# Kernel tuning notes

Hardware: AMD Instinct MI355X
Metric: run time of the kernel (lower is better)

The kernel has to match this reference:

```python
import jax, jax.numpy as jnp
import numpy as np

HIDDEN = 256
BLUR_RADIUS = 3  # truncate gaussian (std=1.0) at 3 sigma -> 7-tap separable kernel


def _gauss_kernel(std=1.0):
    t = jnp.arange(-BLUR_RADIUS, BLUR_RADIUS + 1, dtype=jnp.float32)
    k = jnp.exp(-0.5 * (t / std) ** 2)
    return k / k.sum()


def _blur_axis(vol, k, axis):
    # vol: [B,D,D,D]; separable 1D conv along `axis` (1..3), SAME padding
    v = jnp.moveaxis(vol, axis, -1)
    shp = v.shape
    v = v.reshape(-1, 1, shp[-1])
    out = jax.lax.conv_general_dilated(v, k.reshape(1, 1, -1), (1,), 'SAME')
    return jnp.moveaxis(out.reshape(shp), -1, axis)


def low_pass_3d(vol, std=1.0):
    k = _gauss_kernel(std).astype(vol.dtype)
    for ax in (1, 2, 3):
        vol = _blur_axis(vol, k, ax)
    return vol


def generate_sphere_points(n, rng):
    phi = rng.uniform(0, 2 * np.pi, n)
    cos_theta = rng.uniform(-1, 1, n)
    theta = np.arccos(cos_theta)
    r = rng.uniform(0, 1, n) ** (1.0 / 3.0)
    return np.stack([r * np.sin(theta) * np.cos(phi),
                     r * np.sin(theta) * np.sin(phi),
                     r * np.cos(theta)], axis=-1)


def setup_inputs() -> dict:
    key = jax.random.key(0)
    B, LAT, V, D = 8, 128, 65536, 128
    ks = list(jax.random.split(key, 16))
    rng = np.random.default_rng(0)

    def siren_first(k, fan_in, fan_out):
        lim = 1.0 / fan_in
        return jax.random.uniform(k, (fan_in, fan_out), jnp.float32, -lim, lim)

    def siren(k, fan_in, fan_out, c=6.0):
        lim = np.sqrt(c / fan_in) / 30.0
        return jax.random.uniform(k, (fan_in, fan_out), jnp.float32, -lim, lim)

    def head(k, fan_in, fan_out):
        # variance_scaling(scale=1/3, mode=fan_out, uniform)
        lim = np.sqrt(3.0 * (1.0 / 3.0) / fan_out)
        return jax.random.uniform(k, (fan_in, fan_out), jnp.float32, -lim, lim)

    inp = {
        'x': jax.random.normal(ks[0], (B, LAT), jnp.float32),
        'w0': siren_first(ks[1], LAT, HIDDEN), 'b0': jnp.zeros((HIDDEN,), jnp.float32),
        'w1': siren(ks[2], HIDDEN, HIDDEN), 'b1': jnp.zeros((HIDDEN,), jnp.float32),
        'w2': siren(ks[3], HIDDEN, HIDDEN), 'b2': jnp.zeros((HIDDEN,), jnp.float32),
        'w3': siren(ks[4], HIDDEN, HIDDEN), 'b3': jnp.zeros((HIDDEN,), jnp.float32),
        'w4': siren(ks[5], HIDDEN, HIDDEN), 'b4': jnp.zeros((HIDDEN,), jnp.float32),
        'wc': head(ks[6], HIDDEN, 3 * V), 'bc': jnp.zeros((3 * V,), jnp.float32),
        'wv': head(ks[7], HIDDEN, V), 'bv': jnp.zeros((V,), jnp.float32),
        'coords0': jnp.asarray(0.25 * (generate_sphere_points(V, rng) + rng.normal(0, 0.1, (V, 3))), jnp.float32),
        'values0': jnp.zeros((V,), jnp.float32),
        'volume_size': D,
    }
    return inp


# corner offsets, ordered as in the original concat: 000,100,010,001,011,101,110,111 (x,y,z)
_OFFSETS = jnp.array([[0, 0, 0], [1, 0, 0], [0, 1, 0], [0, 0, 1],
                      [0, 1, 1], [1, 0, 1], [1, 1, 0], [1, 1, 1]], dtype=jnp.int32)


def reference(x, w0, b0, w1, b1, w2, b2, w3, b3, w4, b4, wc, bc, wv, bv,
              coords0, values0, volume_size):
    B = x.shape[0]
    V = values0.shape[0]
    D = volume_size
    factor = 0.5 * D
    bf = jnp.bfloat16

    # --- SIREN MLP (hidden layers computed in bf16, heads in fp32) ---
    h = jnp.sin(30.0 * (x.astype(bf) @ w0.astype(bf) + b0.astype(bf)))
    for w, b in ((w1, b1), (w2, b2), (w3, b3)):
        h = jnp.sin(h + (h @ w.astype(bf) + b.astype(bf)))
    h = h @ w4.astype(bf) + b4.astype(bf)
    h = h.astype(jnp.float32)

    delta_coords = (h @ wc + bc).reshape(B, V, 3)
    values = jax.nn.relu(values0[None, :] + (h @ wv + bv))  # [B,V]

    coords = factor * (coords0[None] + delta_coords) + factor  # [B,V,3], voxel units

    # --- trilinear splatting ---
    bposf = jnp.floor(coords)
    bposi = bposf.astype(jnp.int32)              # [B,V,3]
    f = coords - bposf                           # fractional part, [B,V,3]
    # weight per corner: prod_d (f_d if offset else 1-f_d) -> [B,V,8]
    w8 = jnp.prod(jnp.where(_OFFSETS[None, None].astype(bool), f[:, :, None, :], 1.0 - f[:, :, None, :]), axis=-1)
    amp = values[:, :, None] * w8                # [B,V,8]
    idx = bposi[:, :, None, :] + _OFFSETS[None, None]  # [B,V,8,3] (x,y,z)
    # linear index with (z,y,x) layout as in original scatter
    lin = (idx[..., 2] * D + idx[..., 1]) * D + idx[..., 0]  # [B,V,8]

    def scatter_one(lin_b, amp_b):
        return jnp.zeros((D * D * D,), jnp.float32).at[lin_b.ravel()].add(amp_b.ravel())

    grids = jax.vmap(scatter_one)(lin, amp).reshape(B, D, D, D)

    # --- gaussian low-pass, std=1.0 ---
    grids = low_pass_3d(grids, std=1.0)
    return grids
```

## Files before the change

### kernel.cpp

```cpp
#include <hip/hip_runtime.h>
#include <hip/hip_bf16.h>

#define DD 128
#define D3 (DD*DD*DD)
#define NB 8
#define NV 65536
#define HID 256
#define LAT 128

#define NBIN 2048
#define NBIN_TOT (NBIN*NB)
#define NMASK 512

__device__ __forceinline__ float rbf(float x) {
    unsigned u = __float_as_uint(x);
    unsigned r = (u + 0x7fffu + ((u >> 16) & 1u)) & 0xFFFF0000u;
    return __uint_as_float(r);
}

template<int K, int MODE>
__global__ __launch_bounds__(256) void k_layer(
    const float* __restrict__ in, const float* __restrict__ w,
    const float* __restrict__ bias, float* __restrict__ outp)
{
    __shared__ float in_s[NB * K];
    __shared__ float part[4 * 64 * 8];
    const int tid = threadIdx.x;
    for (int i = tid; i < NB * K; i += 256) in_s[i] = rbf(in[i]);
    __syncthreads();

    const int cl = tid & 63;
    const int ks = tid >> 6;
    const int col = blockIdx.x * 64 + cl;

    float acc[NB];
    #pragma unroll
    for (int b = 0; b < NB; ++b) acc[b] = 0.f;

    const int k0 = ks * (K / 4);
    #pragma unroll 8
    for (int k = k0; k < k0 + K / 4; ++k) {
        float wk = rbf(w[k * HID + col]);
        #pragma unroll
        for (int b = 0; b < NB; ++b) acc[b] = fmaf(in_s[b * K + k], wk, acc[b]);
    }

    float* pp = part + (ks * 64 + cl) * 8;
    #pragma unroll
    for (int b = 0; b < NB; ++b) pp[b] = acc[b];
    __syncthreads();

    #pragma unroll
    for (int u = 0; u < 2; ++u) {
        const int idx = tid * 2 + u;
        const int c2 = idx >> 3, b = idx & 7;
        const int gcol = blockIdx.x * 64 + c2;
        float s = (part[(0 * 64 + c2) * 8 + b] + part[(1 * 64 + c2) * 8 + b])
                + (part[(2 * 64 + c2) * 8 + b] + part[(3 * 64 + c2) * 8 + b]);
        float t = rbf(s);
        t = rbf(t + rbf(bias[gcol]));
        if (MODE == 0) {
            t = rbf(30.0f * t);
            t = rbf(sinf(t));
        } else if (MODE == 1) {
            float r = rbf(in_s[b * K + gcol] + t);
            t = rbf(sinf(r));
        }
        outp[b * HID + gcol] = t;
    }
}

#define PSTR 17
__global__ __launch_bounds__(256, 4) void k_heads(
    const float* __restrict__ h4,
    const float* __restrict__ wc, const float* __restrict__ bc,
    const float* __restrict__ wv, const float* __restrict__ bv,
    const float* __restrict__ coords0, const float* __restrict__ values0,
    float4* __restrict__ posval)
{
    __shared__ float hsT[HID * NB];
    __shared__ __align__(16) char uni[4 * 64 * PSTR * 4];
    float4 (*buf)[512] = reinterpret_cast<float4(*)[512]>(uni);
    float* part = reinterpret_cast<float*>(uni);

    const int tid = threadIdx.x;
    const int blk = blockIdx.x;
    const int p   = tid & 63;
    const int ks  = tid >> 6;

    for (int i = tid; i < NB * HID; i += 256) {
        int b = i >> 8, k = i & 255;
        hsT[k * 8 + b] = h4[b * HID + k];
    }

    const float4* wc4 = reinterpret_cast<const float4*>(wc);
    const float4* wv4 = reinterpret_cast<const float4*>(wv);

    size_t base0, base1, step1;
    {
        int r = tid / 48, c = tid - r * 48;
        base0 = (size_t)((r >> 1) * 64 + (r & 1)) * 49152 + (size_t)blk * 48 + c;
    }
    const float4* src1;
    if (tid < 128) {
        int t1 = tid + 256;
        int r = t1 / 48, c = t1 - r * 48;
        base1 = (size_t)((r >> 1) * 64 + (r & 1)) * 49152 + (size_t)blk * 48 + c;
        src1 = wc4; step1 = 2 * 49152;
    } else {
        int u = tid - 128;
        int r = u >> 4, c = u & 15;
        base1 = (size_t)((r >> 1) * 64 + (r & 1)) * 16384 + (size_t)blk * 16 + c;
        src1 = wv4; step1 = 2 * 16384;
    }
    const size_t step0 = 2 * 49152;
    const int d0 = tid, d1 = tid + 256;

    float acc[4][8];
    #pragma unroll
    for (int c = 0; c < 4; ++c)
        #pragma unroll
        for (int b = 0; b < NB; ++b) acc[c][b] = 0.f;

    const float4* h4v = reinterpret_cast<const float4*>(hsT);

    float4 R0 = wc4[base0];
    float4 R1 = src1[base1];
    buf[0][d0] = R0; buf[0][d1] = R1;
    R0 = wc4[base0 + step0];
    R1 = src1[base1 + step1];
    __syncthreads();

    float4 R0n, R1n;
    for (int s = 0; s < 32; ++s) {
        if (s + 2 < 32) {
            R0n = wc4[base0 + (size_t)(s + 2) * step0];
            R1n = src1[base1 + (size_t)(s + 2) * step1];
        }
        const int bi = s & 1;
        const float* wcsF = reinterpret_cast<const float*>(&buf[bi][0]);
        const float* wvsF = reinterpret_cast<const float*>(&buf[bi][384]);
        #pragma unroll
        for (int j = 0; j < 2; ++j) {
            const int r = ks * 2 + j;
            const int k = ks * 64 + 2 * s + j;
            float c0 = wcsF[r * 192 + 3 * p];
            float c1 = wcsF[r * 192 + 3 * p + 1];
            float c2 = wcsF[r * 192 + 3 * p + 2];
            float vv = wvsF[r * 64 + p];
            float4 hA_ = h4v[k * 2], hB_ = h4v[k * 2 + 1];
            float hb[8] = {hA_.x, hA_.y, hA_.z, hA_.w, hB_.x, hB_.y, hB_.z, hB_.w};
            #pragma unroll
            for (int b = 0; b < NB; ++b) {
                acc[0][b] = fmaf(hb[b], c0, acc[0][b]);
                acc[1][b] = fmaf(hb[b], c1, acc[1][b]);
                acc[2][b] = fmaf(hb[b], c2, acc[2][b]);
                acc[3][b] = fmaf(hb[b], vv, acc[3][b]);
            }
        }
        __syncthreads();
        if (s < 31) {
            buf[bi ^ 1][d0] = R0;
            buf[bi ^ 1][d1] = R1;
            R0 = R0n; R1 = R1n;
            __syncthreads();
        }
    }
    __syncthreads();

    const int bp = ks;
    const int v  = blk * 64 + p;
    const float factor = 0.5f * DD;
    float* pp = part + (ks * 64 + p) * PSTR;

    #pragma unroll
    for (int phase = 0; phase < 2; ++phase) {
        if (phase) __syncthreads();
        #pragma unroll
        for (int q = 0; q < 4; ++q) {
            int b = phase * 4 + q;
            pp[q * 4 + 0] = acc[0][b]; pp[q * 4 + 1] = acc[1][b];
            pp[q * 4 + 2] = acc[2][b]; pp[q * 4 + 3] = acc[3][b];
        }
        __syncthreads();
        {
            const int b = phase * 4 + bp;
            float A0 = 0.f, A1 = 0.f, A2 = 0.f, A3 = 0.f;
            #pragma unroll
            for (int k2 = 0; k2 < 4; ++k2) {
                const float* rp = part + (k2 * 64 + p) * PSTR + bp * 4;
                A0 += rp[0]; A1 += rp[1]; A2 += rp[2]; A3 += rp[3];
            }
            float px = factor * (coords0[3 * v]     + (A0 + bc[3 * v]))     + factor;
            float py = factor * (coords0[3 * v + 1] + (A1 + bc[3 * v + 1])) + factor;
            float pz = factor * (coords0[3 * v + 2] + (A2 + bc[3 * v + 2])) + factor;
            float val = fmaxf(values0[v] + (A3 + bv[v]), 0.f);
            posval[(size_t)b * NV + v] = make_float4(px, py, pz, val);
        }
    }
}

__device__ __forceinline__ bool point_base(float4 q, int& ix, int& iy, int& iz) {
    if (q.w == 0.f) return false;
    ix = (int)floorf(q.x); iy = (int)floorf(q.y); iz = (int)floorf(q.z);
    return ix >= -1 && ix <= 127 && iy >= -1 && iy <= 127 && iz >= -1 && iz <= 127;
}

__device__ __forceinline__ void brick_span(int ix, int iy, int iz,
                                           int& bx0, int& bx1, int& by0, int& by1,
                                           int& bz0, int& bz1) {
    bx0 = (ix < 0 ? 0 : ix) >> 5;  bx1 = (ix + 1 > 127 ? 127 : ix + 1) >> 5;
    by0 = (iy < 0 ? 0 : iy) >> 3;  by1 = (iy + 1 > 127 ? 127 : iy + 1) >> 3;
    bz0 = (iz < 0 ? 0 : iz) >> 2;  bz1 = (iz + 1 > 127 ? 127 : iz + 1) >> 2;
}

__global__ __launch_bounds__(256) void k_count(const float4* __restrict__ posval,
                                               unsigned* __restrict__ binCount,
                                               unsigned* __restrict__ gmask)
{
    __shared__ unsigned hist[NBIN];
    __shared__ unsigned lmask[64];
    const int tid = threadIdx.x;
    const int batch = blockIdx.x >> 5;
    const size_t base = (size_t)batch * NV + (blockIdx.x & 31) * 2048;
    for (int i = tid; i < NBIN; i += 256) hist[i] = 0;
    if (tid < 64) lmask[tid] = 0;
    __syncthreads();
    #pragma unroll
    for (int j = 0; j < 8; ++j) {
        float4 q = posval[base + j * 256 + tid];
        int ix, iy, iz;
        if (point_base(q, ix, iy, iz)) {
            int bx0, bx1, by0, by1, bz0, bz1;
            brick_span(ix, iy, iz, bx0, bx1, by0, by1, bz0, bz1);
            for (int bz = bz0; bz <= bz1; ++bz)
                for (int by = by0; by <= by1; ++by)
                    for (int bx = bx0; bx <= bx1; ++bx)
                        atomicAdd(&hist[(bz * 16 + by) * 4 + bx], 1u);
            int ylo = iy - 3 < 0 ? 0 : iy - 3, yhi = iy + 4 > 127 ? 127 : iy + 4;
            int zlo = iz - 3 < 0 ? 0 : iz - 3, zhi = iz + 4 > 127 ? 127 : iz + 4;
            for (int zc = zlo >> 4; zc <= zhi >> 4; ++zc)
                for (int yc = ylo >> 4; yc <= yhi >> 4; ++yc)
                    lmask[zc * 8 + yc] = 1u;
        }
    }
    __syncthreads();
    for (int i = tid; i < NBIN; i += 256) {
        unsigned c = hist[i];
        if (c) atomicAdd(&binCount[batch * NBIN + i], c);
    }
    if (tid < 64 && lmask[tid]) atomicOr(&gmask[batch * 64 + tid], 1u);
}

__global__ __launch_bounds__(1024) void k_scan(const unsigned* __restrict__ cnt,
                                               unsigned* __restrict__ start,
                                               unsigned* __restrict__ cursor)
{
    __shared__ unsigned partial[1024];
    const int t = threadIdx.x;
    const int base = t * 16;
    unsigned s = 0;
    #pragma unroll
    for (int j = 0; j < 16; ++j) s += cnt[base + j];
    partial[t] = s;
    __syncthreads();
    for (int off = 1; off < 1024; off <<= 1) {
        unsigned mine = partial[t];
        unsigned add = (t >= off) ? partial[t - off] : 0u;
        __syncthreads();
        partial[t] = mine + add;
        __syncthreads();
    }
    unsigned run = (t > 0) ? partial[t - 1] : 0u;
    #pragma unroll
    for (int j = 0; j < 16; ++j) {
        start[base + j] = run;
        cursor[base + j] = run;
        run += cnt[base + j];
    }
    if (t == 1023) start[NBIN_TOT] = partial[1023];
}

__global__ __launch_bounds__(256) void k_scatter(const float4* __restrict__ posval,
                                                 unsigned* __restrict__ binCursor,
                                                 float4* __restrict__ sorted)
{
    __shared__ unsigned hist[NBIN];
    __shared__ unsigned bbase[NBIN];
    const int tid = threadIdx.x;
    const int batch = blockIdx.x >> 5;
    const size_t base = (size_t)batch * NV + (blockIdx.x & 31) * 2048;
    for (int i = tid; i < NBIN; i += 256) hist[i] = 0;
    __syncthreads();

    float4 q[8];
    #pragma unroll
    for (int j = 0; j < 8; ++j) {
        q[j] = posval[base + j * 256 + tid];
        int ix, iy, iz;
        if (point_base(q[j], ix, iy, iz)) {
            int bx0, bx1, by0, by1, bz0, bz1;
            brick_span(ix, iy, iz, bx0, bx1, by0, by1, bz0, bz1);
            for (int bz = bz0; bz <= bz1; ++bz)
                for (int by = by0; by <= by1; ++by)
                    for (int bx = bx0; bx <= bx1; ++bx)
                        atomicAdd(&hist[(bz * 16 + by) * 4 + bx], 1u);
        }
    }
    __syncthreads();
    for (int i = tid; i < NBIN; i += 256) {
        unsigned c = hist[i];
        bbase[i] = c ? atomicAdd(&binCursor[batch * NBIN + i], c) : 0u;
    }
    __syncthreads();
    for (int i = tid; i < NBIN; i += 256) hist[i] = 0;
    __syncthreads();
    #pragma unroll
    for (int j = 0; j < 8; ++j) {
        int ix, iy, iz;
        if (point_base(q[j], ix, iy, iz)) {
            int bx0, bx1, by0, by1, bz0, bz1;
            brick_span(ix, iy, iz, bx0, bx1, by0, by1, bz0, bz1);
            for (int bz = bz0; bz <= bz1; ++bz)
                for (int by = by0; by <= by1; ++by)
                    for (int bx = bx0; bx <= bx1; ++bx) {
                        int bin = (bz * 16 + by) * 4 + bx;
                        unsigned r = atomicAdd(&hist[bin], 1u);
                        sorted[bbase[bin] + r] = q[j];
                    }
        }
    }
}

__global__ __launch_bounds__(256) void k_binsplat(const float4* __restrict__ sorted,
                                                  const unsigned* __restrict__ binStart,
                                                  const unsigned* __restrict__ gmask,
                                                  int maskon,
                                                  float* __restrict__ grid)
{
    __shared__ float brick[4 * 8 * 32];
    const int tid = threadIdx.x;
    const int bid = blockIdx.x;
    const int bx = bid & 3;
    const int by = (bid >> 2) & 15;
    const int bz = (bid >> 6) & 31;
    const int batch = bid >> 11;
    const int x0 = bx << 5, y0 = by << 3, z0 = bz << 2;

    if (maskon && gmask[batch * 64 + (bz >> 2) * 8 + (by >> 1)] == 0u) return;

    const unsigned s = binStart[bid], e = binStart[bid + 1];

    const int vx4 = tid & 7, cy = (tid >> 3) & 7, cz = tid >> 6;
    const size_t o = (size_t)batch * D3 + (size_t)(z0 + cz) * (DD * DD)
                   + (size_t)(y0 + cy) * DD + x0 + vx4 * 4;

    if (s == e) {
        *reinterpret_cast<float4*>(grid + o) = make_float4(0.f, 0.f, 0.f, 0.f);
        return;
    }

    for (int i = tid; i < 1024; i += 256) brick[i] = 0.f;
    __syncthreads();

    for (unsigned i = s + tid; i < e; i += 256) {
        float4 q = sorted[i];
        float fx = floorf(q.x), fy = floorf(q.y), fz = floorf(q.z);
        int vx = (int)fx - x0, vy = (int)fy - y0, vz = (int)fz - z0;
        float gx = q.x - fx, gy = q.y - fy, gz = q.z - fz;
        float wx0 = 1.f - gx, wy0 = 1.f - gy, wz0 = 1.f - gz;
        #pragma unroll
        for (int oz = 0; oz < 2; ++oz)
        #pragma unroll
        for (int oy = 0; oy < 2; ++oy)
        #pragma unroll
        for (int ox = 0; ox < 2; ++ox) {
            int cxx = vx + ox, cyy = vy + oy, czz = vz + oz;
            if ((unsigned)cxx < 32u && (unsigned)cyy < 8u && (unsigned)czz < 4u) {
                float w = ((ox ? gx : wx0) * (oy ? gy : wy0)) * (oz ? gz : wz0);
                atomicAdd(&brick[(czz * 8 + cyy) * 32 + cxx], q.w * w);
            }
        }
    }
    __syncthreads();

    *reinterpret_cast<float4*>(grid + o) =
        *reinterpret_cast<const float4*>(&brick[(cz * 8 + cy) * 32 + vx4 * 4]);
}

__global__ __launch_bounds__(256) void k_blur_z(const float* __restrict__ in,
                                                float* __restrict__ out,
                                                const unsigned* __restrict__ gmask,
                                                int maskon)
{
    const int b = blockIdx.x;
    const int batch = b >> 13;
    const int z = (b >> 6) & 127;
    const int y0 = (b * 2) & 127;
    const long i = (long)b * 256 + threadIdx.x;

    unsigned okbits = 0x7fu;
    if (maskon) {
        if (gmask[batch * 64 + (z >> 4) * 8 + (y0 >> 4)] == 0u) return;
        okbits = 0u;
        #pragma unroll
        for (int j = -3; j <= 3; ++j) {
            int zj = z + j;
            if (zj >= 0 && zj < DD && gmask[batch * 64 + (zj >> 4) * 8 + (y0 >> 4)])
                okbits |= 1u << (j + 3);
        }
    }

    const double e1 = 0.6065306597126334, e2 = 0.1353352832366127, e3 = 0.011108996538242306;
    const double s = 1.0 + 2.0 * (e1 + e2 + e3);
    const float kw[7] = {(float)(e3 / s), (float)(e2 / s), (float)(e1 / s), (float)(1.0 / s),
                         (float)(e1 / s), (float)(e2 / s), (float)(e3 / s)};

    float acc = 0.f;
    #pragma unroll
    for (int j = -3; j <= 3; ++j) {
        int q = z + j;
        if (q >= 0 && q < DD && ((okbits >> (j + 3)) & 1u))
            acc = fmaf(kw[j + 3], in[i + ((long)j << 14)], acc);
    }
    out[i] = acc;
}

__global__ __launch_bounds__(256) void k_blur_yx(const float* __restrict__ in,
                                                 float* __restrict__ out,
                                                 const unsigned* __restrict__ gmask,
                                                 int maskon)
{
    __shared__ float sin_[38 * 128];
    __shared__ float sy[32 * 128];
    __shared__ unsigned mrow[8];

    const double e1 = 0.6065306597126334, e2 = 0.1353352832366127, e3 = 0.011108996538242306;
    const double ss = 1.0 + 2.0 * (e1 + e2 + e3);
    const float kw[7] = {(float)(e3 / ss), (float)(e2 / ss), (float)(e1 / ss), (float)(1.0 / ss),
                         (float)(e1 / ss), (float)(e2 / ss), (float)(e3 / ss)};

    const int tid = threadIdx.x;
    const int bid = blockIdx.x;
    const int ytile = bid & 3;
    const int z = (bid >> 2) & 127;
    const int batch = bid >> 9;
    const int y0 = ytile << 5;
    const size_t slab = (size_t)batch * D3 + (size_t)z * (DD * DD);

    if (maskon) {
        if (tid < 8) mrow[tid] = gmask[batch * 64 + (z >> 4) * 8 + tid];
        __syncthreads();
        const int yc0 = y0 >> 4;
        if (mrow[yc0] == 0u && mrow[yc0 + 1] == 0u) {
            const float4 z4 = make_float4(0.f, 0.f, 0.f, 0.f);
            for (int i = tid; i < 1024; i += 256) {
                int r = i >> 5, xq = i & 31;
                *reinterpret_cast<float4*>(&out[slab + (size_t)(y0 + r) * DD + xq * 4]) = z4;
            }
            return;
        }
    }

    for (int i = tid; i < 38 * 128; i += 256) {
        int row = i >> 7, xx = i & 127;
        int gy = y0 + row - 3;
        bool ok = gy >= 0 && gy < DD && (!maskon || mrow[gy >> 4]);
        sin_[i] = ok ? in[slab + (size_t)gy * DD + xx] : 0.f;
    }
    __syncthreads();

    for (int i = tid; i < 32 * 128; i += 256) {
        int r = i >> 7, xx = i & 127;
        float acc = 0.f;
        #pragma unroll
        for (int j = 0; j < 7; ++j)
            acc = fmaf(kw[j], sin_[(r + j) * 128 + xx], acc);
        sy[i] = acc;
    }
    __syncthreads();

    for (int i = tid; i < 32 * 128; i += 256) {
        int r = i >> 7, xx = i & 127;
        float acc = 0.f;
        #pragma unroll
        for (int j = -3; j <= 3; ++j) {
            int qx = xx + j;
            if (qx >= 0 && qx < DD)
                acc = fmaf(kw[j + 3], sy[r * 128 + qx], acc);
        }
        out[slab + (size_t)(y0 + r) * DD + xx] = acc;
    }
}

extern "C" void kernel_launch(void* const* d_in, const int* in_sizes, int n_in,
                              void* d_out, int out_size, void* d_ws, size_t ws_size,
                              hipStream_t stream) {
    const float* x   = (const float*)d_in[0];
    const float* w0  = (const float*)d_in[1];
    const float* b0  = (const float*)d_in[2];
    const float* w1  = (const float*)d_in[3];
    const float* b1  = (const float*)d_in[4];
    const float* w2  = (const float*)d_in[5];
    const float* b2  = (const float*)d_in[6];
    const float* w3  = (const float*)d_in[7];
    const float* b3  = (const float*)d_in[8];
    const float* w4  = (const float*)d_in[9];
    const float* b4  = (const float*)d_in[10];
    const float* wc  = (const float*)d_in[11];
    const float* bc  = (const float*)d_in[12];
    const float* wv  = (const float*)d_in[13];
    const float* bv  = (const float*)d_in[14];
    const float* c0  = (const float*)d_in[15];
    const float* v0  = (const float*)d_in[16];

    float* out = (float*)d_out;
    float4* posval = (float4*)d_out;
    float* h4 = out + 4 * 1024 * 1024;
    float* hA = h4 + 2048;
    float* hB = hA + 2048;

    const int maskon = (ws_size >= (65ull << 20)) ? 1 : 0;
    const size_t ctrl_off = maskon ? (64ull << 20) : (48ull << 20);
    float4* sorted = (float4*)d_ws;
    unsigned* binCount  = (unsigned*)((char*)d_ws + ctrl_off);
    unsigned* gmask     = binCount + NBIN_TOT;
    unsigned* binStart  = gmask + NMASK;
    unsigned* binCursor = binStart + NBIN_TOT + 1;

    hipMemsetAsync(binCount, 0, (NBIN_TOT + NMASK) * sizeof(unsigned), stream);

    k_layer<LAT, 0><<<4, 256, 0, stream>>>(x,  w0, b0, hA);
    k_layer<HID, 1><<<4, 256, 0, stream>>>(hA, w1, b1, hB);
    k_layer<HID, 1><<<4, 256, 0, stream>>>(hB, w2, b2, hA);
    k_layer<HID, 1><<<4, 256, 0, stream>>>(hA, w3, b3, hB);
    k_layer<HID, 2><<<4, 256, 0, stream>>>(hB, w4, b4, h4);

    k_heads<<<NV / 64, 256, 0, stream>>>(h4, wc, bc, wv, bv, c0, v0, posval);

    k_count<<<256, 256, 0, stream>>>(posval, binCount, gmask);
    k_scan<<<1, 1024, 0, stream>>>(binCount, binStart, binCursor);
    k_scatter<<<256, 256, 0, stream>>>(posval, binCursor, sorted);
    k_binsplat<<<NBIN_TOT, 256, 0, stream>>>(sorted, binStart, gmask, maskon, out);

    const int nblk = (NB * D3) / 256;
    k_blur_z<<<nblk, 256, 0, stream>>>(out, (float*)d_ws, gmask, maskon);
    k_blur_yx<<<NB * 512, 256, 0, stream>>>((float*)d_ws, out, gmask, maskon);
}
```

Before: 306.3 us.

## Triple-buffer heads weight staging and widen MLP layer blocks to 1024 threads

The heads kernel moves from a double-buffered shared-memory weight pipeline with two barriers per step to a triple-buffered rotation with a single custom barrier per step. The custom barrier waits on lgkmcnt and adds a scheduling fence. The MLP layer kernels now use 1024 threads, splitting the K dimension 16 ways instead of 4, with a padded partial-sum buffer. The aim is to cut sync overhead and latency in small serial kernels, at the cost of more LDS and a longer reduction.

```diff
diff --git a/kernel.cpp b/kernel.cpp
--- a/kernel.cpp
+++ b/kernel.cpp
@@ -19,14 +19,14 @@
 }
 
 template<int K, int MODE>
-__global__ __launch_bounds__(256) void k_layer(
+__global__ __launch_bounds__(1024) void k_layer(
     const float* __restrict__ in, const float* __restrict__ w,
     const float* __restrict__ bias, float* __restrict__ outp)
 {
     __shared__ float in_s[NB * K];
-    __shared__ float part[4 * 64 * 8];
+    __shared__ float part[16 * 64 * 9];
     const int tid = threadIdx.x;
-    for (int i = tid; i < NB * K; i += 256) in_s[i] = rbf(in[i]);
+    for (int i = tid; i < NB * K; i += 1024) in_s[i] = rbf(in[i]);
     __syncthreads();
 
     const int cl = tid & 63;
@@ -37,26 +37,25 @@
     #pragma unroll
     for (int b = 0; b < NB; ++b) acc[b] = 0.f;
 
-    const int k0 = ks * (K / 4);
+    const int k0 = ks * (K / 16);
     #pragma unroll 8
-    for (int k = k0; k < k0 + K / 4; ++k) {
+    for (int k = k0; k < k0 + K / 16; ++k) {
         float wk = rbf(w[k * HID + col]);
         #pragma unroll
         for (int b = 0; b < NB; ++b) acc[b] = fmaf(in_s[b * K + k], wk, acc[b]);
     }
 
-    float* pp = part + (ks * 64 + cl) * 8;
+    float* pp = part + (ks * 64 + cl) * 9;
     #pragma unroll
     for (int b = 0; b < NB; ++b) pp[b] = acc[b];
     __syncthreads();
 
-    #pragma unroll
-    for (int u = 0; u < 2; ++u) {
-        const int idx = tid * 2 + u;
-        const int c2 = idx >> 3, b = idx & 7;
+    if (tid < 512) {
+        const int c2 = tid >> 3, b = tid & 7;
         const int gcol = blockIdx.x * 64 + c2;
-        float s = (part[(0 * 64 + c2) * 8 + b] + part[(1 * 64 + c2) * 8 + b])
-                + (part[(2 * 64 + c2) * 8 + b] + part[(3 * 64 + c2) * 8 + b]);
+        float s = 0.f;
+        #pragma unroll
+        for (int kk = 0; kk < 16; ++kk) s += part[(kk * 64 + c2) * 9 + b];
         float t = rbf(s);
         t = rbf(t + rbf(bias[gcol]));
         if (MODE == 0) {
@@ -79,7 +78,7 @@
     float4* __restrict__ posval)
 {
     __shared__ float hsT[HID * NB];
-    __shared__ __align__(16) char uni[4 * 64 * PSTR * 4];
+    __shared__ __align__(16) char uni[3 * 512 * 16];
     float4 (*buf)[512] = reinterpret_cast<float4(*)[512]>(uni);
     float* part = reinterpret_cast<float*>(uni);
 
@@ -124,48 +123,76 @@
 
     const float4* h4v = reinterpret_cast<const float4*>(hsT);
 
-    float4 R0 = wc4[base0];
-    float4 R1 = src1[base1];
-    buf[0][d0] = R0; buf[0][d1] = R1;
-    R0 = wc4[base0 + step0];
-    R1 = src1[base1 + step1];
-    __syncthreads();
-
-    float4 R0n, R1n;
-    for (int s = 0; s < 32; ++s) {
-        if (s + 2 < 32) {
-            R0n = wc4[base0 + (size_t)(s + 2) * step0];
-            R1n = src1[base1 + (size_t)(s + 2) * step1];
-        }
-        const int bi = s & 1;
-        const float* wcsF = reinterpret_cast<const float*>(&buf[bi][0]);
-        const float* wvsF = reinterpret_cast<const float*>(&buf[bi][384]);
-        #pragma unroll
-        for (int j = 0; j < 2; ++j) {
-            const int r = ks * 2 + j;
-            const int k = ks * 64 + 2 * s + j;
-            float c0 = wcsF[r * 192 + 3 * p];
-            float c1 = wcsF[r * 192 + 3 * p + 1];
-            float c2 = wcsF[r * 192 + 3 * p + 2];
-            float vv = wvsF[r * 64 + p];
-            float4 hA_ = h4v[k * 2], hB_ = h4v[k * 2 + 1];
-            float hb[8] = {hA_.x, hA_.y, hA_.z, hA_.w, hB_.x, hB_.y, hB_.z, hB_.w};
-            #pragma unroll
-            for (int b = 0; b < NB; ++b) {
-                acc[0][b] = fmaf(hb[b], c0, acc[0][b]);
-                acc[1][b] = fmaf(hb[b], c1, acc[1][b]);
-                acc[2][b] = fmaf(hb[b], c2, acc[2][b]);
-                acc[3][b] = fmaf(hb[b], vv, acc[3][b]);
+    #define SBAR() do { \
+        asm volatile("s_waitcnt lgkmcnt(0)" ::: "memory"); \
+        __builtin_amdgcn_s_barrier(); \
+        __builtin_amdgcn_sched_barrier(0); \
+    } while (0)
+
+    #define COMPUTE(s_, bi_) { \
+        const float* wcsF = reinterpret_cast<const float*>(&buf[bi_][0]); \
+        const float* wvsF = reinterpret_cast<const float*>(&buf[bi_][384]); \
+        _Pragma("unroll") \
+        for (int j = 0; j < 2; ++j) { \
+            const int r = ks * 2 + j; \
+            const int k = ks * 64 + 2 * (s_) + j; \
+            float c0 = wcsF[r * 192 + 3 * p]; \
+            float c1 = wcsF[r * 192 + 3 * p + 1]; \
+            float c2 = wcsF[r * 192 + 3 * p + 2]; \
+            float vv = wvsF[r * 64 + p]; \
+            float4 hA_ = h4v[k * 2], hB_ = h4v[k * 2 + 1]; \
+            float hb[8] = {hA_.x, hA_.y, hA_.z, hA_.w, hB_.x, hB_.y, hB_.z, hB_.w}; \
+            _Pragma("unroll") \
+            for (int b = 0; b < NB; ++b) { \
+                acc[0][b] = fmaf(hb[b], c0, acc[0][b]); \
+                acc[1][b] = fmaf(hb[b], c1, acc[1][b]); \
+                acc[2][b] = fmaf(hb[b], c2, acc[2][b]); \
+                acc[3][b] = fmaf(hb[b], vv, acc[3][b]); \
+            } \
+        } \
+    }
+
+    float4 Ra0, Ra1, Rb0, Rb1, Rc0, Rc1;
+    Ra0 = wc4[base0];                 Ra1 = src1[base1];
+    Rb0 = wc4[base0 + step0];         Rb1 = src1[base1 + step1];
+    Rc0 = wc4[base0 + 2 * step0];     Rc1 = src1[base1 + 2 * step1];
+    buf[0][d0] = Ra0; buf[0][d1] = Ra1;
+    SBAR();
+
+    for (int t = 0; t < 11; ++t) {
+        {
+            const int s = 3 * t;
+            COMPUTE(s, 0);
+            if (s <= 30) { buf[1][d0] = Rb0; buf[1][d1] = Rb1; }
+            if (s <= 28) {
+                Ra0 = wc4[base0 + (size_t)(s + 3) * step0];
+                Ra1 = src1[base1 + (size_t)(s + 3) * step1];
             }
-        }
-        __syncthreads();
-        if (s < 31) {
-            buf[bi ^ 1][d0] = R0;
-            buf[bi ^ 1][d1] = R1;
-            R0 = R0n; R1 = R1n;
-            __syncthreads();
-        }
-    }
+            SBAR();
+        }
+        if (3 * t + 1 < 32) {
+            const int s = 3 * t + 1;
+            COMPUTE(s, 1);
+            if (s <= 30) { buf[2][d0] = Rc0; buf[2][d1] = Rc1; }
+            if (s <= 28) {
+                Rb0 = wc4[base0 + (size_t)(s + 3) * step0];
+                Rb1 = src1[base1 + (size_t)(s + 3) * step1];
+            }
+            SBAR();
+        }
+        if (3 * t + 2 < 32) {
+            const int s = 3 * t + 2;
+            COMPUTE(s, 2);
+            if (s <= 30) { buf[0][d0] = Ra0; buf[0][d1] = Ra1; }
+            if (s <= 28) {
+                Rc0 = wc4[base0 + (size_t)(s + 3) * step0];
+                Rc1 = src1[base1 + (size_t)(s + 3) * step1];
+            }
+            SBAR();
+        }
+    }
+    #undef COMPUTE
+    #undef SBAR
     __syncthreads();
 
     const int bp = ks;
@@ -530,11 +557,11 @@
 
     hipMemsetAsync(binCount, 0, (NBIN_TOT + NMASK) * sizeof(unsigned), stream);
 
-    k_layer<LAT, 0><<<4, 256, 0, stream>>>(x,  w0, b0, hA);
-    k_layer<HID, 1><<<4, 256, 0, stream>>>(hA, w1, b1, hB);
-    k_layer<HID, 1><<<4, 256, 0, stream>>>(hB, w2, b2, hA);
-    k_layer<HID, 1><<<4, 256, 0, stream>>>(hA, w3, b3, hB);
-    k_layer<HID, 2><<<4, 256, 0, stream>>>(hB, w4, b4, h4);
+    k_layer<LAT, 0><<<4, 1024, 0, stream>>>(x,  w0, b0, hA);
+    k_layer<HID, 1><<<4, 1024, 0, stream>>>(hA, w1, b1, hB);
+    k_layer<HID, 1><<<4, 1024, 0, stream>>>(hB, w2, b2, hA);
+    k_layer<HID, 1><<<4, 1024, 0, stream>>>(hA, w3, b3, hB);
+    k_layer<HID, 2><<<4, 1024, 0, stream>>>(hB, w4, b4, h4);
 
     k_heads<<<NV / 64, 256, 0, stream>>>(h4, wc, bc, wv, bv, c0, v0, posval);
 
```

Result: faster. 293.3 us (-4.2%).
